# Kernel optimization log

Hardware: AMD Instinct MI355X
Metric: run time of the kernel (lower is better)

The kernel has to match this reference:

```python
import jax, jax.numpy as jnp
import numpy as np

IMG = 512
B = 4
NA = 3          # anchors per location
NC = 3          # classes
K = 512         # pre-NMS top-k per image per level (<= smallest level anchor count 768)
STRIDES = [4, 8, 16, 32]
MIN_S = [0.01, 0.02, 0.03, 0.04]
MAX_S = [0.06, 0.08, 0.10, 0.12]
W_SC = [0.8, 0.9, 1.0, 1.1]
H_SC = [1.0, 1.2, 1.4, 1.6]
CONF_T = 0.15
NMS_T = 0.5
STD = 0.2       # box_delta_stds (means are 0)


def make_anchors(stride):
    H = IMG // stride
    c = (np.arange(H) + 0.5) * stride
    cy, cx = np.meshgrid(c, c, indexing='ij')           # [H, W]
    sizes = stride * 4.0 * (2.0 ** (np.arange(NA) / 3.0))  # [A]
    cx = np.broadcast_to(cx, (NA, H, H))
    cy = np.broadcast_to(cy, (NA, H, H))
    s = sizes[:, None, None]
    # A-major, then H, W -- matches permute(0,1,3,4,2).reshape flattening
    anc = np.stack([cx - s / 2, cy - s / 2, cx + s / 2, cy + s / 2], -1).reshape(-1, 4)
    return jnp.asarray(anc, jnp.float32)


def setup_inputs() -> dict:
    key = jax.random.key(0)
    ks = jax.random.split(key, 8)
    inp = {}
    for l, s in enumerate(STRIDES):
        H = IMG // s
        inp[f'cls{l}'] = jax.random.normal(ks[2 * l], (B, NA, NC, H, H), jnp.float32)
        inp[f'box{l}'] = jax.random.normal(ks[2 * l + 1], (B, NA, 4, H, H), jnp.float32)
        inp[f'anc{l}'] = make_anchors(s)
    inp['image_size'] = IMG
    return inp


def decode_level(cls, box, anc, lvl, image_size):
    Bc, A, C, H, W = cls.shape
    scores = jax.nn.sigmoid(jnp.transpose(cls, (0, 1, 3, 4, 2)).reshape(Bc, -1, C))  # [B,N,C]
    d = jnp.transpose(box, (0, 1, 3, 4, 2)).reshape(Bc, -1, 4)                        # [B,N,4]
    img = jnp.asarray(image_size, jnp.float32)
    aw = (anc[:, 2] - anc[:, 0]) / img
    ah = (anc[:, 3] - anc[:, 1]) / img
    acx = (anc[:, 0] + anc[:, 2]) * 0.5 / img
    acy = (anc[:, 1] + anc[:, 3]) * 0.5 / img
    fs = 1.0 / STRIDES[lvl]
    dx = jnp.clip(d[..., 0] * STD, -1.0, 1.0) * fs * aw
    dy = jnp.clip(d[..., 1] * STD, -1.0, 1.0) * fs * ah
    cx = jnp.clip(acx + dx, 0.0, 1.0)
    cy = jnp.clip(acy + dy, 0.0, 1.0)
    dw = jnp.clip(d[..., 2] * STD, -2.0, 2.0)
    dh = jnp.clip(d[..., 3] * STD, -2.0, 2.0)
    pw = jnp.clip(aw * W_SC[lvl] * jnp.exp(dw * (0.2 + 0.1 * lvl)), MIN_S[lvl] * 0.8, MAX_S[lvl] * 0.9)
    ph = jnp.clip(ah * H_SC[lvl] * jnp.exp(dh * (0.4 + 0.2 * lvl)), MIN_S[lvl] * 0.8, MAX_S[lvl] * 1.2)
    boxes = jnp.stack([
        jnp.clip(cx - 0.5 * pw, 0.0, 1.0),
        jnp.clip(cy - 0.5 * ph, 0.0, 1.0),
        jnp.clip(cx + 0.5 * pw, 0.0, 1.0),
        jnp.clip(cy + 0.5 * ph, 0.0, 1.0)], -1)                                       # [B,N,4]
    ms = scores.max(-1)
    mc = scores.argmax(-1)
    w = boxes[..., 2] - boxes[..., 0]
    h = boxes[..., 3] - boxes[..., 1]
    valid = (ms > CONF_T) & (w > MIN_S[lvl] * 0.5) & (h > MIN_S[lvl] * 0.5) \
            & (w < MAX_S[lvl] * 2.0) & (h < MAX_S[lvl] * 2.0)
    # pre-NMS top-k on (masked) scores
    sort_key = jnp.where(valid, ms, -1.0)
    _, idx = jax.lax.top_k(sort_key, K)                                               # [B,K]
    boxes_k = jnp.take_along_axis(boxes, idx[..., None], 1)
    scores_k = jnp.take_along_axis(ms, idx, 1)
    labels_k = jnp.take_along_axis(mc, idx, 1)
    valid_k = jnp.take_along_axis(valid, idx, 1)
    return boxes_k, scores_k, labels_k, valid_k


def pairwise_iou(b):
    area = (b[:, 2] - b[:, 0]) * (b[:, 3] - b[:, 1])
    lt = jnp.maximum(b[:, None, :2], b[None, :, :2])
    rb = jnp.minimum(b[:, None, 2:], b[None, :, 2:])
    wh = jnp.clip(rb - lt, 0.0)
    inter = wh[..., 0] * wh[..., 1]
    return inter / (area[:, None] + area[None, :] - inter + 1e-9)


def nms_keep(boxes, valid):
    # boxes sorted by descending score; sequential greedy NMS
    iou = pairwise_iou(boxes)                 # [K,K]
    rank = jnp.arange(K)
    def body(i, keep):
        overlap = jnp.max(jnp.where((rank < i) & keep, iou[i], 0.0))
        return keep.at[i].set(valid[i] & (overlap <= NMS_T))
    return jax.lax.fori_loop(0, K, body, jnp.zeros((K,), bool))


def reference(cls0, box0, anc0, cls1, box1, anc1, cls2, box2, anc2, cls3, box3, anc3, image_size):
    levels = [(cls0, box0, anc0), (cls1, box1, anc1), (cls2, box2, anc2), (cls3, box3, anc3)]
    outs = [decode_level(c, b, a, l, image_size) for l, (c, b, a) in enumerate(levels)]
    boxes = jnp.stack([o[0] for o in outs], 1)    # [B, L, K, 4]
    scores = jnp.stack([o[1] for o in outs], 1)   # [B, L, K]
    labels = jnp.stack([o[2] for o in outs], 1)   # [B, L, K]
    valid = jnp.stack([o[3] for o in outs], 1)    # [B, L, K]
    keep = jax.vmap(jax.vmap(nms_keep))(boxes, valid)
    boxes = jnp.where(keep[..., None], boxes, 0.0)
    scores = jnp.where(keep, scores, 0.0)
    labels = jnp.where(keep, labels + 1, 0)       # torch code returns labels + 1
    return boxes, scores, labels, keep
```

## Files before the change

### kernel.cpp

```cpp
#include <hip/hip_runtime.h>
#include <math.h>

#define K_TOP 512
#define CAND_CAP 3072

struct LvlC {
  int H, lgH, HH, lgHH;
  float fs, wsc, hsc, wex, hex, pwlo, pwhi, phlo, phhi, minwh, maxwh;
};

__device__ const LvlC LVL[4] = {
  {128, 7, 16384, 14, 0.25f,    0.8f, 1.0f, 0.2f, 0.4f, 0.008f, 0.054f, 0.008f, 0.072f, 0.005f, 0.12f},
  { 64, 6,  4096, 12, 0.125f,   0.9f, 1.2f, 0.3f, 0.6f, 0.016f, 0.072f, 0.016f, 0.096f, 0.01f,  0.16f},
  { 32, 5,  1024, 10, 0.0625f,  1.0f, 1.4f, 0.4f, 0.8f, 0.024f, 0.09f,  0.024f, 0.12f,  0.015f, 0.2f },
  { 16, 4,   256,  8, 0.03125f, 1.1f, 1.6f, 0.5f, 1.0f, 0.032f, 0.108f, 0.032f, 0.144f, 0.02f,  0.24f},
};

__device__ const float TSEL[4] = {0.91f, 0.85f, 0.65f, -2.0f};

__device__ __forceinline__ void decode_box(const LvlC& L, const float* __restrict__ boxp,
                                           const float* __restrict__ ancp,
                                           int b, int idx, float rimg,
                                           float& x0, float& y0, float& x1, float& y1)
{
#pragma clang fp contract(off)
  int a   = idx >> L.lgHH;
  int rem = idx & (L.HH - 1);
  const float* bp = boxp + (size_t)((b * 3 + a) * 4) * L.HH + rem;
  float d0 = bp[0], d1 = bp[L.HH], d2 = bp[2 * L.HH], d3 = bp[3 * L.HH];
  float4 av = reinterpret_cast<const float4*>(ancp)[idx];
  float a0 = av.x, a1 = av.y, a2 = av.z, a3 = av.w;
  float aw  = (a2 - a0) * rimg;
  float ah  = (a3 - a1) * rimg;
  float acx = (a0 + a2) * 0.5f * rimg;
  float acy = (a1 + a3) * 0.5f * rimg;
  float dx = fminf(fmaxf(d0 * 0.2f, -1.f), 1.f) * L.fs * aw;
  float dy = fminf(fmaxf(d1 * 0.2f, -1.f), 1.f) * L.fs * ah;
  float cx = fminf(fmaxf(acx + dx, 0.f), 1.f);
  float cy = fminf(fmaxf(acy + dy, 0.f), 1.f);
  float dw = fminf(fmaxf(d2 * 0.2f, -2.f), 2.f);
  float dh = fminf(fmaxf(d3 * 0.2f, -2.f), 2.f);
  float pw = fminf(fmaxf(aw * L.wsc * expf(dw * L.wex), L.pwlo), L.pwhi);
  float ph = fminf(fmaxf(ah * L.hsc * expf(dh * L.hex), L.phlo), L.phhi);
  x0 = fminf(fmaxf(cx - 0.5f * pw, 0.f), 1.f);
  y0 = fminf(fmaxf(cy - 0.5f * ph, 0.f), 1.f);
  x1 = fminf(fmaxf(cx + 0.5f * pw, 0.f), 1.f);
  y1 = fminf(fmaxf(cy + 0.5f * ph, 0.f), 1.f);
}

__device__ __forceinline__ void seg_map(int blk, int& b, int& l, int& base, int& iblk)
{
  b = blk / 255;
  int rb = blk - b * 255;
  if (rb < 192)      { l = 0; iblk = rb;       base = 0;     }
  else if (rb < 240) { l = 1; iblk = rb - 192; base = 49152; }
  else if (rb < 252) { l = 2; iblk = rb - 240; base = 61440; }
  else               { l = 3; iblk = rb - 252; base = 64512; }
}

__global__ __launch_bounds__(256) void dc_kernel(
    const float* __restrict__ cls0, const float* __restrict__ box0, const float* __restrict__ anc0,
    const float* __restrict__ cls1, const float* __restrict__ box1, const float* __restrict__ anc1,
    const float* __restrict__ cls2, const float* __restrict__ box2, const float* __restrict__ anc2,
    const float* __restrict__ cls3, const float* __restrict__ box3, const float* __restrict__ anc3,
    const int* __restrict__ imgp, unsigned long long* __restrict__ keys,
    unsigned long long* __restrict__ cand, unsigned* __restrict__ unitCnt)
{
  __shared__ unsigned wcnt[4];
  int unit = (int)blockIdx.x;
  int tid = (int)threadIdx.x;
  int wid = tid >> 6, lane = tid & 63;
  int b, l, base, iblk;
  seg_map(unit, b, l, base, iblk);
  int i = iblk * 256 + tid;

  const float *cls, *boxp, *ancp;
  switch (l) {
    case 0:  cls = cls0; boxp = box0; ancp = anc0; break;
    case 1:  cls = cls1; boxp = box1; ancp = anc1; break;
    case 2:  cls = cls2; boxp = box2; ancp = anc2; break;
    default: cls = cls3; boxp = box3; ancp = anc3; break;
  }
  LvlC L = LVL[l];
  float rimg = 1.0f / (float)(*imgp);

  int a   = i >> L.lgHH;
  int rem = i & (L.HH - 1);
  const float* cp = cls + (size_t)((b * 3 + a) * 3) * L.HH + rem;
  float c0 = cp[0], c1 = cp[L.HH], c2 = cp[2 * L.HH];
  float m = c0; int mc = 0;
  if (c1 > m) { m = c1; mc = 1; }
  if (c2 > m) { m = c2; mc = 2; }
  float ms = 1.f / (1.f + expf(-m));

  float x0, y0, x1, y1;
  decode_box(L, boxp, ancp, b, i, rimg, x0, y0, x1, y1);
  float w = x1 - x0, h = y1 - y0;
  bool valid = (ms > 0.15f) && (w > L.minwh) && (h > L.minwh) && (w < L.maxwh) && (h < L.maxwh);

  float sk = valid ? ms : -1.0f;
  unsigned u = __float_as_uint(sk);
  unsigned ascu  = (u & 0x80000000u) ? ~u : (u | 0x80000000u);
  unsigned descu = ~ascu;
  unsigned long long key = ((unsigned long long)descu << 32)
                         | ((unsigned long long)(unsigned)i << 16)
                         | ((unsigned)mc << 8) | (valid ? 1u : 0u);
  keys[(size_t)b * 65280 + base + i] = key;

  bool take = (sk >= TSEL[l]);
  unsigned long long bm = __ballot(take);
  if (lane == 0) wcnt[wid] = (unsigned)__popcll(bm);
  __syncthreads();
  if (take) {
    unsigned off = 0;
    for (int w2 = 0; w2 < wid; ++w2) off += wcnt[w2];
    off += (unsigned)__popcll(bm & ((1ull << lane) - 1ull));
    cand[(size_t)unit * 256 + off] = key;
  }
  if (tid == 0) unitCnt[unit] = wcnt[0] + wcnt[1] + wcnt[2] + wcnt[3];
}

__global__ __launch_bounds__(512) void selmask_kernel(
    const unsigned long long* __restrict__ keys,
    const unsigned long long* __restrict__ cand, const unsigned* __restrict__ unitCnt,
    const float* __restrict__ box0, const float* __restrict__ anc0,
    const float* __restrict__ box1, const float* __restrict__ anc1,
    const float* __restrict__ box2, const float* __restrict__ anc2,
    const float* __restrict__ box3, const float* __restrict__ anc3,
    const int* __restrict__ imgp,
    float* __restrict__ boxesWS, float* __restrict__ scoresWS,
    int* __restrict__ labelsWS, unsigned* __restrict__ validWS,
    unsigned long long* __restrict__ masks)
{
  union SelU {
    unsigned long long scand[CAND_CAP];
    float4 sBox[K_TOP];
  };
  __shared__ SelU su;
  __shared__ unsigned long long skey[K_TOP];
  __shared__ unsigned long long skey2[K_TOP];
  __shared__ unsigned hist[8][256];
  __shared__ unsigned upref[256];
  __shared__ unsigned ucnt_s[256];
  __shared__ unsigned waveSum[8];
  __shared__ unsigned long long shPrefix;
  __shared__ unsigned shBelow, shCnt, shTotal;

  int blk = (int)blockIdx.x;
  int seg = blk >> 5;
  int sub = blk & 31;
  int b = seg >> 2, l = seg & 3;
  int tid = (int)threadIdx.x;
  const int nt = 512;
  int wid = tid >> 6, lane = tid & 63;

  const int nArr[4]    = {49152, 12288, 3072, 768};
  const int baseArr[4] = {0, 49152, 61440, 64512};
  const int nuArr[4]   = {192, 48, 12, 3};
  const int fuArr[4]   = {0, 192, 240, 252};
  int N = nArr[l];
  int nu = nuArr[l];
  int firstU = b * 255 + fuArr[l];
  const unsigned long long* kp = keys + (size_t)b * 65280 + baseArr[l];

  if (tid == 0) { shPrefix = 0ull; shBelow = 0u; shCnt = 0u; }

  unsigned c = (tid < nu) ? unitCnt[firstU + tid] : 0u;
  if (tid < 256) ucnt_s[tid] = c;
  unsigned incl = c;
  for (int off = 1; off < 64; off <<= 1) {
    unsigned n = __shfl_up(incl, off);
    if (lane >= off) incl += n;
  }
  if (lane == 63) waveSum[wid] = incl;
  __syncthreads();
  if (tid < 256) {
    unsigned add = 0;
    for (int w2 = 0; w2 < wid; ++w2) add += waveSum[w2];
    if (tid < nu) upref[tid] = incl - c + add;
  }
  if (tid == 0) shTotal = waveSum[0] + waveSum[1] + waveSum[2] + waveSum[3];
  __syncthreads();

  unsigned total = shTotal;
  bool useCand = (total >= K_TOP && total <= CAND_CAP);
  int M = useCand ? (int)total : N;

  if (useCand) {
    for (int f = tid; f < (int)total; f += nt) {
      int lo = 0, hi = nu - 1;
      while (lo < hi) {
        int mid = (lo + hi + 1) >> 1;
        if ((int)upref[mid] <= f) lo = mid; else hi = mid - 1;
      }
      su.scand[f] = cand[(size_t)(firstU + lo) * 256 + (unsigned)(f - (int)upref[lo])];
    }
  }
  __syncthreads();

  for (int r = 0; r < 6; ++r) {
    int shift = 56 - 8 * r;
    for (int v = tid; v < 8 * 256; v += nt) ((unsigned*)hist)[v] = 0u;
    __syncthreads();
    unsigned long long pref = shPrefix;
    unsigned below = shBelow;
    unsigned long long hiMask = (r == 0) ? 0ull : (~0ull << (64 - 8 * r));
    for (int t = tid; t < M; t += nt) {
      unsigned long long k = useCand ? su.scand[t] : kp[t];
      if ((k & hiMask) == (pref & hiMask))
        atomicAdd(&hist[wid][(unsigned)((k >> shift) & 0xFF)], 1u);
    }
    __syncthreads();
    unsigned s = 0, incl2 = 0;
    if (tid < 256) {
#pragma unroll
      for (int w2 = 0; w2 < 8; ++w2) s += hist[w2][tid];
      incl2 = s;
    }
    for (int off = 1; off < 64; off <<= 1) {
      unsigned n = __shfl_up(incl2, off);
      if (lane >= off) incl2 += n;
    }
    if (lane == 63) waveSum[wid] = incl2;
    __syncthreads();
    if (tid < 256) {
      unsigned add = 0;
      for (int w2 = 0; w2 < wid; ++w2) add += waveSum[w2];
      unsigned inclT = incl2 + add;
      unsigned exclT = inclT - s;
      if (below + exclT < K_TOP && below + inclT >= K_TOP) {
        shBelow = below + exclT;
        shPrefix = pref | ((unsigned long long)(unsigned)tid << shift);
      }
    }
    __syncthreads();
  }
  unsigned long long kth = shPrefix | 0xFFFFull;

  for (int t = tid; t < M; t += nt) {
    unsigned long long k = useCand ? su.scand[t] : kp[t];
    bool take = (k <= kth);
    unsigned long long bm = __ballot(take);
    unsigned bp = 0;
    if (lane == 0 && bm) bp = atomicAdd(&shCnt, (unsigned)__popcll(bm));
    bp = __shfl(bp, 0);
    if (take) skey[bp + (unsigned)__popcll(bm & ((1ull << lane) - 1ull))] = k;
  }
  __syncthreads();

  {
    unsigned long long mykey = skey[tid];
    int rank = 0;
#pragma unroll 8
    for (int j = 0; j < K_TOP; ++j) rank += (skey[j] < mykey) ? 1 : 0;
    skey2[rank] = mykey;
  }
  __syncthreads();

  unsigned long long key = skey2[tid];
  __syncthreads();

  const float *boxp, *ancp;
  switch (l) {
    case 0:  boxp = box0; ancp = anc0; break;
    case 1:  boxp = box1; ancp = anc1; break;
    case 2:  boxp = box2; ancp = anc2; break;
    default: boxp = box3; ancp = anc3; break;
  }
  LvlC L = LVL[l];
  float rimg = 1.0f / (float)(*imgp);
  {
    int idx = (int)((key >> 16) & 0xFFFFull);
    unsigned descu = (unsigned)(key >> 32);
    unsigned ascu  = ~descu;
    unsigned u = (ascu & 0x80000000u) ? (ascu & 0x7FFFFFFFu) : ~ascu;
    float x0, y0, x1, y1;
    decode_box(L, boxp, ancp, b, idx, rimg, x0, y0, x1, y1);
    float4 bb; bb.x = x0; bb.y = y0; bb.z = x1; bb.w = y1;
    su.sBox[tid] = bb;
    if (sub == 0) {
      int o = seg * K_TOP + tid;
      reinterpret_cast<float4*>(boxesWS)[o] = bb;
      scoresWS[o] = __uint_as_float(u);
      labelsWS[o] = (int)((key >> 8) & 0xFFull);
      validWS[o]  = (unsigned)(key & 1ull);
    }
  }
  __syncthreads();

  {
#pragma clang fp contract(off)
    unsigned long long* mseg = masks + (size_t)seg * K_TOP * 8;
    float4 bj[8]; float aj[8];
#pragma unroll
    for (int cc = 0; cc < 8; ++cc) {
      bj[cc] = su.sBox[cc * 64 + lane];
      aj[cc] = (bj[cc].z - bj[cc].x) * (bj[cc].w - bj[cc].y);
    }
#pragma unroll
    for (int rr = 0; rr < 2; ++rr) {
      int r = sub * 16 + wid * 2 + rr;
      float4 br = su.sBox[r];
      float ar_ = (br.z - br.x) * (br.w - br.y);
#pragma unroll
      for (int cc = 0; cc < 8; ++cc) {
        float ltx = fmaxf(br.x, bj[cc].x), lty = fmaxf(br.y, bj[cc].y);
        float rbx = fminf(br.z, bj[cc].z), rby = fminf(br.w, bj[cc].w);
        float ww = fmaxf(rbx - ltx, 0.f), hh = fmaxf(rby - lty, 0.f);
        float inter = ww * hh;
        float iou = inter / (ar_ + aj[cc] - inter + 1e-9f);
        unsigned long long bal = __ballot(iou > 0.5f);
        if (lane == 0) mseg[cc * K_TOP + r] = bal;
      }
    }
  }
}

__global__ __launch_bounds__(512) void scan_kernel(
    const unsigned long long* __restrict__ masks,
    const float* __restrict__ boxesWS, const float* __restrict__ scoresWS,
    const int* __restrict__ labelsWS, const unsigned* __restrict__ validWS,
    float* __restrict__ out)
{
  __shared__ unsigned long long sMaskT[8 * K_TOP];
  __shared__ unsigned long long keepWords[8];
  __shared__ unsigned sChanged;

  int seg = (int)blockIdx.x;
  int tid = (int)threadIdx.x;
  int wid = tid >> 6, lane = tid & 63;
  const unsigned long long* mp = masks + (size_t)seg * K_TOP * 8;
#pragma unroll
  for (int w = 0; w < 8; ++w) sMaskT[w * K_TOP + tid] = mp[w * K_TOP + tid];
  bool valid = validWS[seg * K_TOP + tid] != 0u;

  unsigned long long myWord = __ballot(valid);
  if (lane == 0) keepWords[wid] = myWord;
  __syncthreads();

  for (int it = 0; it < 513; ++it) {
    unsigned long long sup = 0ull;
    for (int w = 0; w < wid; ++w)
      sup |= sMaskT[w * K_TOP + tid] & keepWords[w];
    sup |= sMaskT[wid * K_TOP + tid] & keepWords[wid] & ((1ull << lane) - 1ull);
    bool nk = valid && (sup == 0ull);
    unsigned long long nw = __ballot(nk);
    __syncthreads();
    if (tid == 0) sChanged = 0u;
    __syncthreads();
    if (lane == 0) {
      if (nw != keepWords[wid]) sChanged = 1u;
      keepWords[wid] = nw;
    }
    __syncthreads();
    if (sChanged == 0u) break;
  }

  int o = seg * K_TOP + tid;
  bool keep = (keepWords[wid] >> lane) & 1ull;
  float4 bx = reinterpret_cast<const float4*>(boxesWS)[o];
  float4 ob;
  ob.x = keep ? bx.x : 0.f;
  ob.y = keep ? bx.y : 0.f;
  ob.z = keep ? bx.z : 0.f;
  ob.w = keep ? bx.w : 0.f;
  reinterpret_cast<float4*>(out)[o] = ob;
  out[32768 + o] = keep ? scoresWS[o] : 0.f;
  out[40960 + o] = keep ? (float)(labelsWS[o] + 1) : 0.f;
  out[49152 + o] = keep ? 1.f : 0.f;
}

extern "C" void kernel_launch(void* const* d_in, const int* in_sizes, int n_in,
                              void* d_out, int out_size, void* d_ws, size_t ws_size,
                              hipStream_t stream)
{
  const float* cls0 = (const float*)d_in[0];
  const float* box0 = (const float*)d_in[1];
  const float* anc0 = (const float*)d_in[2];
  const float* cls1 = (const float*)d_in[3];
  const float* box1 = (const float*)d_in[4];
  const float* anc1 = (const float*)d_in[5];
  const float* cls2 = (const float*)d_in[6];
  const float* box2 = (const float*)d_in[7];
  const float* anc2 = (const float*)d_in[8];
  const float* cls3 = (const float*)d_in[9];
  const float* box3 = (const float*)d_in[10];
  const float* anc3 = (const float*)d_in[11];
  const int*   imgp = (const int*)d_in[12];

  char* ws = (char*)d_ws;
  unsigned long long* keys    = (unsigned long long*)(ws + 0);
  unsigned long long* cand    = (unsigned long long*)(ws + 2088960);
  unsigned*           unitCnt = (unsigned*)(ws + 4177920);
  float*              boxesWS = (float*)(ws + 4182016);
  float*              scoresWS= (float*)(ws + 4313088);
  int*                labelsWS= (int*)(ws + 4345856);
  unsigned*           validWS = (unsigned*)(ws + 4378624);
  unsigned long long* masks   = (unsigned long long*)(ws + 4411392);
  float* out = (float*)d_out;

  dc_kernel<<<1020, 256, 0, stream>>>(cls0, box0, anc0, cls1, box1, anc1,
                                      cls2, box2, anc2, cls3, box3, anc3,
                                      imgp, keys, cand, unitCnt);
  selmask_kernel<<<512, 512, 0, stream>>>(keys, cand, unitCnt,
                                          box0, anc0, box1, anc1, box2, anc2, box3, anc3,
                                          imgp, boxesWS, scoresWS, labelsWS, validWS, masks);
  scan_kernel<<<16, 512, 0, stream>>>(masks, boxesWS, scoresWS, labelsWS, validWS, out);
}
```

Measured before the change: 120.2 us.

## Fuse NMS scan into selection kernel via last-block-done atomic counter

The separate scan kernel is removed. Each of the 32 blocks per segment bumps a per-segment done counter after writing its IoU mask rows, and the last block to finish runs the greedy keep-scan and writes the outputs straight from its own registers and shared memory. This drops one kernel launch and the boxes/scores/labels/valid workspace round trip. In exchange it adds atomics, fences and a larger shared-memory union, and the scan now runs on only 16 late-finishing blocks.

```diff
diff --git a/kernel.cpp b/kernel.cpp
--- a/kernel.cpp
+++ b/kernel.cpp
@@ -64,12 +64,16 @@
     const float* __restrict__ cls2, const float* __restrict__ box2, const float* __restrict__ anc2,
     const float* __restrict__ cls3, const float* __restrict__ box3, const float* __restrict__ anc3,
     const int* __restrict__ imgp, unsigned long long* __restrict__ keys,
-    unsigned long long* __restrict__ cand, unsigned* __restrict__ unitCnt)
+    unsigned long long* __restrict__ cand, unsigned* __restrict__ unitCnt,
+    unsigned* __restrict__ segDone)
 {
   __shared__ unsigned wcnt[4];
   int unit = (int)blockIdx.x;
   int tid = (int)threadIdx.x;
   int wid = tid >> 6, lane = tid & 63;
+
+  if (unit == 0 && tid < 16) segDone[tid * 16] = 0u;
+
   int b, l, base, iblk;
   seg_map(unit, b, l, base, iblk);
   int i = iblk * 256 + tid;
@@ -120,7 +124,7 @@
   if (tid == 0) unitCnt[unit] = wcnt[0] + wcnt[1] + wcnt[2] + wcnt[3];
 }
 
-__global__ __launch_bounds__(512) void selmask_kernel(
+__global__ __launch_bounds__(512) void selmaskscan_kernel(
     const unsigned long long* __restrict__ keys,
     const unsigned long long* __restrict__ cand, const unsigned* __restrict__ unitCnt,
     const float* __restrict__ box0, const float* __restrict__ anc0,
@@ -128,23 +132,27 @@
     const float* __restrict__ box2, const float* __restrict__ anc2,
     const float* __restrict__ box3, const float* __restrict__ anc3,
     const int* __restrict__ imgp,
-    float* __restrict__ boxesWS, float* __restrict__ scoresWS,
-    int* __restrict__ labelsWS, unsigned* __restrict__ validWS,
-    unsigned long long* __restrict__ masks)
+    unsigned long long* __restrict__ masks, unsigned* __restrict__ segDone,
+    float* __restrict__ out)
 {
-  union SelU {
-    unsigned long long scand[CAND_CAP];
-    float4 sBox[K_TOP];
+  union BigU {
+    struct {
+      unsigned long long scand[CAND_CAP];
+      unsigned hist[8][256];
+    } a;
+    unsigned long long sMaskT[8 * K_TOP];
   };
-  __shared__ SelU su;
+  __shared__ BigU bu;
+  __shared__ float4 sBox[K_TOP];
   __shared__ unsigned long long skey[K_TOP];
   __shared__ unsigned long long skey2[K_TOP];
-  __shared__ unsigned hist[8][256];
   __shared__ unsigned upref[256];
   __shared__ unsigned ucnt_s[256];
   __shared__ unsigned waveSum[8];
   __shared__ unsigned long long shPrefix;
-  __shared__ unsigned shBelow, shCnt, shTotal;
+  __shared__ unsigned shBelow, shCnt, shTotal, shLast;
+  __shared__ unsigned long long keepWords[8];
+  __shared__ unsigned sChanged;
 
   int blk = (int)blockIdx.x;
   int seg = blk >> 5;
@@ -193,28 +201,28 @@
         int mid = (lo + hi + 1) >> 1;
         if ((int)upref[mid] <= f) lo = mid; else hi = mid - 1;
       }
-      su.scand[f] = cand[(size_t)(firstU + lo) * 256 + (unsigned)(f - (int)upref[lo])];
+      bu.a.scand[f] = cand[(size_t)(firstU + lo) * 256 + (unsigned)(f - (int)upref[lo])];
     }
   }
   __syncthreads();
 
   for (int r = 0; r < 6; ++r) {
     int shift = 56 - 8 * r;
-    for (int v = tid; v < 8 * 256; v += nt) ((unsigned*)hist)[v] = 0u;
+    for (int v = tid; v < 8 * 256; v += nt) ((unsigned*)bu.a.hist)[v] = 0u;
     __syncthreads();
     unsigned long long pref = shPrefix;
     unsigned below = shBelow;
     unsigned long long hiMask = (r == 0) ? 0ull : (~0ull << (64 - 8 * r));
     for (int t = tid; t < M; t += nt) {
-      unsigned long long k = useCand ? su.scand[t] : kp[t];
+      unsigned long long k = useCand ? bu.a.scand[t] : kp[t];
       if ((k & hiMask) == (pref & hiMask))
-        atomicAdd(&hist[wid][(unsigned)((k >> shift) & 0xFF)], 1u);
+        atomicAdd(&bu.a.hist[wid][(unsigned)((k >> shift) & 0xFF)], 1u);
     }
     __syncthreads();
     unsigned s = 0, incl2 = 0;
     if (tid < 256) {
 #pragma unroll
-      for (int w2 = 0; w2 < 8; ++w2) s += hist[w2][tid];
+      for (int w2 = 0; w2 < 8; ++w2) s += bu.a.hist[w2][tid];
       incl2 = s;
     }
     for (int off = 1; off < 64; off <<= 1) {
@@ -238,7 +246,7 @@
   unsigned long long kth = shPrefix | 0xFFFFull;
 
   for (int t = tid; t < M; t += nt) {
-    unsigned long long k = useCand ? su.scand[t] : kp[t];
+    unsigned long long k = useCand ? bu.a.scand[t] : kp[t];
     bool take = (k <= kth);
     unsigned long long bm = __ballot(take);
     unsigned bp = 0;
@@ -257,9 +265,6 @@
   }
   __syncthreads();
 
-  unsigned long long key = skey2[tid];
-  __syncthreads();
-
   const float *boxp, *ancp;
   switch (l) {
     case 0:  boxp = box0; ancp = anc0; break;
@@ -269,22 +274,20 @@
   }
   LvlC L = LVL[l];
   float rimg = 1.0f / (float)(*imgp);
+  float myScore; int myLabel; bool myValid;
   {
+    unsigned long long key = skey2[tid];
     int idx = (int)((key >> 16) & 0xFFFFull);
     unsigned descu = (unsigned)(key >> 32);
     unsigned ascu  = ~descu;
     unsigned u = (ascu & 0x80000000u) ? (ascu & 0x7FFFFFFFu) : ~ascu;
+    myScore = __uint_as_float(u);
+    myLabel = (int)((key >> 8) & 0xFFull);
+    myValid = (key & 1ull) != 0ull;
     float x0, y0, x1, y1;
     decode_box(L, boxp, ancp, b, idx, rimg, x0, y0, x1, y1);
     float4 bb; bb.x = x0; bb.y = y0; bb.z = x1; bb.w = y1;
-    su.sBox[tid] = bb;
-    if (sub == 0) {
-      int o = seg * K_TOP + tid;
-      reinterpret_cast<float4*>(boxesWS)[o] = bb;
-      scoresWS[o] = __uint_as_float(u);
-      labelsWS[o] = (int)((key >> 8) & 0xFFull);
-      validWS[o]  = (unsigned)(key & 1ull);
-    }
+    sBox[tid] = bb;
   }
   __syncthreads();
 
@@ -294,13 +297,13 @@
     float4 bj[8]; float aj[8];
 #pragma unroll
     for (int cc = 0; cc < 8; ++cc) {
-      bj[cc] = su.sBox[cc * 64 + lane];
+      bj[cc] = sBox[cc * 64 + lane];
       aj[cc] = (bj[cc].z - bj[cc].x) * (bj[cc].w - bj[cc].y);
     }
 #pragma unroll
     for (int rr = 0; rr < 2; ++rr) {
       int r = sub * 16 + wid * 2 + rr;
-      float4 br = su.sBox[r];
+      float4 br = sBox[r];
       float ar_ = (br.z - br.x) * (br.w - br.y);
 #pragma unroll
       for (int cc = 0; cc < 8; ++cc) {
@@ -310,40 +313,43 @@
         float inter = ww * hh;
         float iou = inter / (ar_ + aj[cc] - inter + 1e-9f);
         unsigned long long bal = __ballot(iou > 0.5f);
-        if (lane == 0) mseg[cc * K_TOP + r] = bal;
+        if (lane == 0)
+          __hip_atomic_store(&mseg[cc * K_TOP + r], bal,
+                             __ATOMIC_RELAXED, __HIP_MEMORY_SCOPE_AGENT);
       }
     }
   }
-}
-
-__global__ __launch_bounds__(512) void scan_kernel(
-    const unsigned long long* __restrict__ masks,
-    const float* __restrict__ boxesWS, const float* __restrict__ scoresWS,
-    const int* __restrict__ labelsWS, const unsigned* __restrict__ validWS,
-    float* __restrict__ out)
-{
-  __shared__ unsigned long long sMaskT[8 * K_TOP];
-  __shared__ unsigned long long keepWords[8];
-  __shared__ unsigned sChanged;
-
-  int seg = (int)blockIdx.x;
-  int tid = (int)threadIdx.x;
-  int wid = tid >> 6, lane = tid & 63;
-  const unsigned long long* mp = masks + (size_t)seg * K_TOP * 8;
+  __syncthreads();
+
+  if (tid == 0) {
+    __threadfence();
+    unsigned old = __hip_atomic_fetch_add(&segDone[seg * 16], 1u,
+                                          __ATOMIC_ACQ_REL, __HIP_MEMORY_SCOPE_AGENT);
+    shLast = (old == 31u) ? 1u : 0u;
+  }
+  __syncthreads();
+  if (shLast == 0u) return;
+  if (tid == 0) __threadfence();
+  __syncthreads();
+
+  {
+    const unsigned long long* mseg = masks + (size_t)seg * K_TOP * 8;
 #pragma unroll
-  for (int w = 0; w < 8; ++w) sMaskT[w * K_TOP + tid] = mp[w * K_TOP + tid];
-  bool valid = validWS[seg * K_TOP + tid] != 0u;
-
-  unsigned long long myWord = __ballot(valid);
+    for (int w = 0; w < 8; ++w)
+      bu.sMaskT[w * K_TOP + tid] = __hip_atomic_load(&mseg[w * K_TOP + tid],
+                                                     __ATOMIC_RELAXED, __HIP_MEMORY_SCOPE_AGENT);
+  }
+
+  unsigned long long myWord = __ballot(myValid);
   if (lane == 0) keepWords[wid] = myWord;
   __syncthreads();
 
   for (int it = 0; it < 513; ++it) {
     unsigned long long sup = 0ull;
     for (int w = 0; w < wid; ++w)
-      sup |= sMaskT[w * K_TOP + tid] & keepWords[w];
-    sup |= sMaskT[wid * K_TOP + tid] & keepWords[wid] & ((1ull << lane) - 1ull);
-    bool nk = valid && (sup == 0ull);
+      sup |= bu.sMaskT[w * K_TOP + tid] & keepWords[w];
+    sup |= bu.sMaskT[wid * K_TOP + tid] & keepWords[wid] & ((1ull << lane) - 1ull);
+    bool nk = myValid && (sup == 0ull);
     unsigned long long nw = __ballot(nk);
     __syncthreads();
     if (tid == 0) sChanged = 0u;
@@ -356,18 +362,20 @@
     if (sChanged == 0u) break;
   }
 
-  int o = seg * K_TOP + tid;
-  bool keep = (keepWords[wid] >> lane) & 1ull;
-  float4 bx = reinterpret_cast<const float4*>(boxesWS)[o];
-  float4 ob;
-  ob.x = keep ? bx.x : 0.f;
-  ob.y = keep ? bx.y : 0.f;
-  ob.z = keep ? bx.z : 0.f;
-  ob.w = keep ? bx.w : 0.f;
-  reinterpret_cast<float4*>(out)[o] = ob;
-  out[32768 + o] = keep ? scoresWS[o] : 0.f;
-  out[40960 + o] = keep ? (float)(labelsWS[o] + 1) : 0.f;
-  out[49152 + o] = keep ? 1.f : 0.f;
+  {
+    int o = seg * K_TOP + tid;
+    bool keep = (keepWords[wid] >> lane) & 1ull;
+    float4 bx = sBox[tid];
+    float4 ob;
+    ob.x = keep ? bx.x : 0.f;
+    ob.y = keep ? bx.y : 0.f;
+    ob.z = keep ? bx.z : 0.f;
+    ob.w = keep ? bx.w : 0.f;
+    reinterpret_cast<float4*>(out)[o] = ob;
+    out[32768 + o] = keep ? myScore : 0.f;
+    out[40960 + o] = keep ? (float)(myLabel + 1) : 0.f;
+    out[49152 + o] = keep ? 1.f : 0.f;
+  }
 }
 
 extern "C" void kernel_launch(void* const* d_in, const int* in_sizes, int n_in,
@@ -392,18 +400,14 @@
   unsigned long long* keys    = (unsigned long long*)(ws + 0);
   unsigned long long* cand    = (unsigned long long*)(ws + 2088960);
   unsigned*           unitCnt = (unsigned*)(ws + 4177920);
-  float*              boxesWS = (float*)(ws + 4182016);
-  float*              scoresWS= (float*)(ws + 4313088);
-  int*                labelsWS= (int*)(ws + 4345856);
-  unsigned*           validWS = (unsigned*)(ws + 4378624);
-  unsigned long long* masks   = (unsigned long long*)(ws + 4411392);
+  unsigned long long* masks   = (unsigned long long*)(ws + 4182016);
+  unsigned*           segDone = (unsigned*)(ws + 4706304);
   float* out = (float*)d_out;
 
   dc_kernel<<<1020, 256, 0, stream>>>(cls0, box0, anc0, cls1, box1, anc1,
                                       cls2, box2, anc2, cls3, box3, anc3,
-                                      imgp, keys, cand, unitCnt);
-  selmask_kernel<<<512, 512, 0, stream>>>(keys, cand, unitCnt,
-                                          box0, anc0, box1, anc1, box2, anc2, box3, anc3,
-                                          imgp, boxesWS, scoresWS, labelsWS, validWS, masks);
-  scan_kernel<<<16, 512, 0, stream>>>(masks, boxesWS, scoresWS, labelsWS, validWS, out);
+                                      imgp, keys, cand, unitCnt, segDone);
+  selmaskscan_kernel<<<512, 512, 0, stream>>>(keys, cand, unitCnt,
+                                              box0, anc0, box1, anc1, box2, anc2, box3, anc3,
+                                              imgp, masks, segDone, out);
 }
```

Result: slower. 141.1 us (+17.4%).
